# Kernel tuning notes

Measured on AMD Instinct MI355X. Metric: run time of the kernel, lower is better.

## Reference

```python
import jax, jax.numpy as jnp
import numpy as np
import math

N_HEADS = 12  # from init_kwargs


def setup_inputs() -> dict:
    key = jax.random.key(0)
    ks = jax.random.split(key, 9)
    B, N, D = 32, 577, 768
    s = 1.0 / math.sqrt(D)
    return {
        "x": jax.random.normal(ks[0], (B, N, D), jnp.float32),
        "Wq": jax.random.normal(ks[1], (D, D), jnp.float32) * s,
        "bq": jax.random.normal(ks[2], (D,), jnp.float32) * 0.02,
        "Wk": jax.random.normal(ks[3], (D, D), jnp.float32) * s,
        "bk": jax.random.normal(ks[4], (D,), jnp.float32) * 0.02,
        "Wv": jax.random.normal(ks[5], (D, D), jnp.float32) * s,
        "bv": jax.random.normal(ks[6], (D,), jnp.float32) * 0.02,
        "Wo": jax.random.normal(ks[7], (D, D), jnp.float32) * s,
        "bo": jax.random.normal(ks[8], (D,), jnp.float32) * 0.02,
    }


def reference(x, Wq, bq, Wk, bk, Wv, bv, Wo, bo):
    B, N, D = x.shape
    H = N_HEADS
    Hd = D // H
    # project then split heads (intended semantics of the torch module)
    q = (x @ Wq.T + bq).reshape(B, N, H, Hd)
    k = (x @ Wk.T + bk).reshape(B, N, H, Hd)
    v = (x @ Wv.T + bv).reshape(B, N, H, Hd)
    # NOTE: faithful quirk - scale by sqrt(d_size), not sqrt(head_dim)
    scores = jnp.einsum('bqhd,bkhd->bhqk', q, k) / math.sqrt(D)  # [B,H,N,N]
    # faithful quirk: mask = triu(ones); positions where mask==0 (strictly
    # lower triangle, k < q) are filled with float32 min -> anti-causal mask
    allowed = jnp.triu(jnp.ones((N, N), dtype=bool))
    scores = jnp.where(allowed, scores, jnp.finfo(jnp.float32).min)
    att = jax.nn.softmax(scores, axis=3)  # dropout p=0.0 -> identity
    out = jnp.einsum('bhqk,bkhd->bqhd', att, v).reshape(B, N, D)
    return out @ Wo.T + bo
```

## Files before the change

### kernel.cpp

```cpp
#include <hip/hip_runtime.h>
#include <cstdint>
#include <cstddef>


typedef __bf16 bf16;
typedef __bf16 bf16x4 __attribute__((ext_vector_type(4)));
typedef __bf16 bf16x8 __attribute__((ext_vector_type(8)));
typedef float  f32x4  __attribute__((ext_vector_type(4)));

#define DEVI __device__ __forceinline__

constexpr int BATCH = 32;
constexpr int NSEQ  = 577;
constexpr int DMODEL= 768;
constexpr int NHEAD = 12;
constexpr int HD    = 64;
constexpr int M_ROWS = BATCH * NSEQ;
constexpr int M_PAD  = 145 * 128;
constexpr int N_PAD  = 640;
constexpr int QKV_N  = 3 * DMODEL;
constexpr float QSCALE = 0.036084391824351615f * 1.4426950408889634f;

DEVI void async_copy16(const void* g, void* l) {
  void* gg = (void*)(uintptr_t)g;
  __builtin_amdgcn_global_load_lds(
      (__attribute__((address_space(1))) void*)gg,
      (__attribute__((address_space(3))) void*)l,
      16, 0, 0);
}

DEVI f32x4 mfma16(bf16x8 a, bf16x8 b, f32x4 c) {
  return __builtin_amdgcn_mfma_f32_16x16x32_bf16(a, b, c, 0, 0, 0);
}

__global__ __launch_bounds__(256) void cast_kernel(
    const float* __restrict__ x,
    const float* __restrict__ wq, const float* __restrict__ wk,
    const float* __restrict__ wv, const float* __restrict__ wo,
    bf16* __restrict__ xb, bf16* __restrict__ wcat, bf16* __restrict__ wob)
{
  constexpr int XQ = (M_ROWS * DMODEL) / 4;
  constexpr int WQ = (DMODEL * DMODEL) / 4;
  int idx = blockIdx.x * 256 + threadIdx.x;
  const float4* src; bf16* dst; int off;
  if (idx < XQ) { src = (const float4*)x; dst = xb; off = idx; }
  else {
    int u = idx - XQ; int w = u / WQ; off = u - w * WQ;
    src = (const float4*)(w == 0 ? wq : w == 1 ? wk : w == 2 ? wv : wo);
    dst = (w < 3) ? (wcat + (size_t)w * DMODEL * DMODEL) : wob;
  }
  float4 v = src[off];
  bf16x4 o;
  o[0] = (bf16)v.x; o[1] = (bf16)v.y; o[2] = (bf16)v.z; o[3] = (bf16)v.w;
  *(bf16x4*)(dst + (size_t)off * 4) = o;
}

template <int MODE>
__global__ __launch_bounds__(256) void gemm_bt(
    const bf16* __restrict__ A, const bf16* __restrict__ Bw,
    const float* __restrict__ bias0, const float* __restrict__ bias1,
    const float* __restrict__ bias2,
    float* __restrict__ Cout,
    bf16* __restrict__ Qb, bf16* __restrict__ Kb, bf16* __restrict__ Vtb)
{
  __shared__ __align__(16) bf16 As[128 * 64];
  __shared__ __align__(16) bf16 Bs[128 * 64];
  const int t = threadIdx.x;
  const int w = t >> 6, lane = t & 63;
  const int g = lane >> 4, cl = lane & 15;
  const int wm = (w >> 1) * 64, wn = (w & 1) * 64;
  const int m0 = blockIdx.y * 128, n0 = blockIdx.x * 128;

  f32x4 acc[4][4] = {};

  const int srow = t >> 3;
  const int scol = ((t & 7) ^ (srow & 7)) * 8;
  const bf16* Ag = A  + (size_t)(m0 + srow) * 768 + scol;
  const bf16* Bg = Bw + (size_t)(n0 + srow) * 768 + scol;
  char* lA = (char*)As + w * 1024;
  char* lB = (char*)Bs + w * 1024;

  for (int kb = 0; kb < 768; kb += 64) {
#pragma unroll
    for (int c = 0; c < 4; ++c) {
      async_copy16(Ag + kb + (size_t)c * 32 * 768, lA + c * 4096);
      async_copy16(Bg + kb + (size_t)c * 32 * 768, lB + c * 4096);
    }
    __syncthreads();
#pragma unroll
    for (int ks = 0; ks < 2; ++ks) {
      const int ch = ((ks * 4 + g) ^ (cl & 7)) * 8;
      bf16x8 af[4], bfr[4];
#pragma unroll
      for (int i = 0; i < 4; ++i)
        af[i] = *(const bf16x8*)(As + (wm + i * 16 + cl) * 64 + ch);
#pragma unroll
      for (int j = 0; j < 4; ++j)
        bfr[j] = *(const bf16x8*)(Bs + (wn + j * 16 + cl) * 64 + ch);
#pragma unroll
      for (int i = 0; i < 4; ++i)
#pragma unroll
        for (int j = 0; j < 4; ++j)
          acc[i][j] = mfma16(af[i], bfr[j], acc[i][j]);
    }
    __syncthreads();
  }

  if constexpr (MODE == 0) {
#pragma unroll
    for (int j = 0; j < 4; ++j) {
      const int n = n0 + wn + j * 16 + cl;
      const int which = n >= 1536 ? 2 : (n >= 768 ? 1 : 0);
      const int rem = n - which * 768;
      const int h = rem >> 6, d = rem & 63;
      const float bias = (which == 0 ? bias0 : which == 1 ? bias1 : bias2)[rem];
#pragma unroll
      for (int i = 0; i < 4; ++i) {
#pragma unroll
        for (int r = 0; r < 4; ++r) {
          const unsigned m = (unsigned)(m0 + wm + i * 16 + g * 4 + r);
          if (m >= (unsigned)M_ROWS) continue;
          const unsigned bb = m / 577u;
          const unsigned nq = m - bb * 577u;
          const float fv = acc[i][j][r] + bias;
          if (which == 0)
            Qb[((size_t)(bb * NHEAD + h) * N_PAD + nq) * HD + d] = (bf16)(fv * QSCALE);
          else if (which == 1)
            Kb[((size_t)(bb * NHEAD + h) * N_PAD + nq) * HD + d] = (bf16)fv;
          else
            Vtb[((size_t)(bb * NHEAD + h) * HD + d) * N_PAD + nq] = (bf16)fv;
        }
      }
    }
  } else {
#pragma unroll
    for (int j = 0; j < 4; ++j) {
      const int n = n0 + wn + j * 16 + cl;
      const float bias = bias0[n];
#pragma unroll
      for (int i = 0; i < 4; ++i) {
#pragma unroll
        for (int r = 0; r < 4; ++r) {
          const unsigned m = (unsigned)(m0 + wm + i * 16 + g * 4 + r);
          if (m < (unsigned)M_ROWS)
            Cout[(size_t)m * 768 + n] = acc[i][j][r] + bias;
        }
      }
    }
  }
}

__global__ __launch_bounds__(256) void attn_kernel(
    const bf16* __restrict__ Qb, const bf16* __restrict__ Kb,
    const bf16* __restrict__ Vtb, bf16* __restrict__ Ao)
{
  __shared__ __align__(16) bf16 Qs[64 * 64];
  __shared__ __align__(16) bf16 Ks[64 * 64];
  __shared__ __align__(16) bf16 Vs[64 * 64];
  __shared__ __align__(16) bf16 Ps[4 * 16 * 64];

  const int t = threadIdx.x, w = t >> 6, lane = t & 63;
  const int g = lane >> 4, cl = lane & 15;
  const int qb = blockIdx.x;
  const int bh = blockIdx.y;
  const size_t kqbase = (size_t)bh * (N_PAD * HD);
  const size_t vbase  = (size_t)bh * (HD * N_PAD);

  const int srow = t >> 3;
  const int scol = ((t & 7) ^ (srow & 7)) * 8;

  {
    const bf16* Qg = Qb + kqbase + (size_t)(qb * 64 + srow) * HD + scol;
    async_copy16(Qg,           (char*)Qs + w * 1024);
    async_copy16(Qg + 32 * HD, (char*)Qs + 4096 + w * 1024);
  }

  f32x4 oacc[4] = {};
  f32x4 lsum = {};
  bf16x8 onesf;
#pragma unroll
  for (int e = 0; e < 8; ++e) onesf[e] = (bf16)(cl == 0 ? 1.0f : 0.0f);

  const int q0 = qb * 64 + w * 16 + g * 4;
  const bf16* Kg = Kb  + kqbase + (size_t)srow * HD + scol;
  const bf16* Vg = Vtb + vbase  + (size_t)srow * N_PAD + scol;
  bf16* pw = Ps + w * 1024;

  for (int jb = qb; jb < 10; ++jb) {
    async_copy16(Kg + (size_t)jb * 64 * HD,            (char*)Ks + w * 1024);
    async_copy16(Kg + (size_t)(jb * 64 + 32) * HD,     (char*)Ks + 4096 + w * 1024);
    async_copy16(Vg + jb * 64,                         (char*)Vs + w * 1024);
    async_copy16(Vg + jb * 64 + (size_t)32 * N_PAD,    (char*)Vs + 4096 + w * 1024);
    __syncthreads();

    f32x4 s[4] = {};
#pragma unroll
    for (int ks = 0; ks < 2; ++ks) {
      const int ch = ((ks * 4 + g) ^ (cl & 7)) * 8;
      bf16x8 aq = *(const bf16x8*)(Qs + (w * 16 + cl) * 64 + ch);
#pragma unroll
      for (int j = 0; j < 4; ++j) {
        bf16x8 bk = *(const bf16x8*)(Ks + (j * 16 + cl) * 64 + ch);
        s[j] = mfma16(aq, bk, s[j]);
      }
    }

    float p[4][4];
    if (jb == qb || jb == 9) {
#pragma unroll
      for (int j = 0; j < 4; ++j) {
        const int kg = jb * 64 + j * 16 + cl;
#pragma unroll
        for (int r = 0; r < 4; ++r) {
          const bool ok = (kg >= q0 + r) && (kg < NSEQ);
          p[j][r] = ok ? exp2f(s[j][r]) : 0.f;
        }
      }
    } else {
#pragma unroll
      for (int j = 0; j < 4; ++j)
#pragma unroll
        for (int r = 0; r < 4; ++r)
          p[j][r] = exp2f(s[j][r]);
    }

#pragma unroll
    for (int j = 0; j < 4; ++j)
#pragma unroll
      for (int r = 0; r < 4; ++r) {
        const int row = g * 4 + r;
        const int col = j * 16 + cl;
        pw[row * 64 + ((col >> 3) ^ (row & 7)) * 8 + (col & 7)] = (bf16)p[j][r];
      }

#pragma unroll
    for (int ks = 0; ks < 2; ++ks) {
      const int ch = ((ks * 4 + g) ^ (cl & 7)) * 8;
      bf16x8 ap = *(const bf16x8*)(pw + cl * 64 + ch);
#pragma unroll
      for (int j = 0; j < 4; ++j) {
        bf16x8 bv = *(const bf16x8*)(Vs + (j * 16 + cl) * 64 + ch);
        oacc[j] = mfma16(ap, bv, oacc[j]);
      }
      lsum = mfma16(ap, onesf, lsum);
    }
    __syncthreads();
  }

  const int b_ = bh / NHEAD, h_ = bh - (bh / NHEAD) * NHEAD;
#pragma unroll
  for (int r = 0; r < 4; ++r) {
    const int qg = q0 + r;
    const float l = __shfl(lsum[r], lane & 48, 64);
    if (qg >= NSEQ) continue;
    const float inv = 1.f / l;
    const size_t row = ((size_t)b_ * NSEQ + qg) * DMODEL + h_ * HD;
#pragma unroll
    for (int j = 0; j < 4; ++j)
      Ao[row + j * 16 + cl] = (bf16)(oacc[j][r] * inv);
  }
}

extern "C" void kernel_launch(void* const* d_in, const int* in_sizes, int n_in,
                              void* d_out, int out_size, void* d_ws, size_t ws_size,
                              hipStream_t stream) {
  const float* x  = (const float*)d_in[0];
  const float* Wq = (const float*)d_in[1];
  const float* bq = (const float*)d_in[2];
  const float* Wk = (const float*)d_in[3];
  const float* bk = (const float*)d_in[4];
  const float* Wv = (const float*)d_in[5];
  const float* bv = (const float*)d_in[6];
  const float* Wo = (const float*)d_in[7];
  const float* bo = (const float*)d_in[8];

  char* ws = (char*)d_ws;
  size_t off = 0;
  auto alloc = [&](size_t bytes) -> char* {
    char* p = ws + off;
    off += (bytes + 255) & ~(size_t)255;
    return p;
  };
  bf16* xb   = (bf16*)alloc((size_t)M_PAD * DMODEL * 2);
  bf16* wcat = (bf16*)alloc((size_t)QKV_N * DMODEL * 2);
  bf16* wob  = (bf16*)alloc((size_t)DMODEL * DMODEL * 2);
  bf16* Qb   = (bf16*)alloc((size_t)BATCH * NHEAD * N_PAD * HD * 2);
  bf16* Kb   = (bf16*)alloc((size_t)BATCH * NHEAD * N_PAD * HD * 2);
  bf16* Vtb  = (bf16*)alloc((size_t)BATCH * NHEAD * HD * N_PAD * 2);
  bf16* Ao   = (bf16*)alloc((size_t)M_PAD * DMODEL * 2);
  (void)ws_size; (void)in_sizes; (void)n_in; (void)out_size;

  constexpr int XQ = (M_ROWS * DMODEL) / 4;
  constexpr int WQ = (DMODEL * DMODEL) / 4;
  const int cast_blocks = (XQ + 4 * WQ) / 256;
  cast_kernel<<<cast_blocks, 256, 0, stream>>>(x, Wq, Wk, Wv, Wo, xb, wcat, wob);

  gemm_bt<0><<<dim3(QKV_N / 128, M_PAD / 128), 256, 0, stream>>>(
      xb, wcat, bq, bk, bv, nullptr, Qb, Kb, Vtb);

  attn_kernel<<<dim3(10, BATCH * NHEAD), 256, 0, stream>>>(Qb, Kb, Vtb, Ao);

  gemm_bt<1><<<dim3(DMODEL / 128, M_PAD / 128), 256, 0, stream>>>(
      Ao, wob, bo, nullptr, nullptr, (float*)d_out, nullptr, nullptr, nullptr);
}
```

Measured before the change: 400.3 us.

## Use 128-query attention tiles with double-buffered K/V and halve GEMM K-step

```diff
diff --git a/kernel.cpp b/kernel.cpp
--- a/kernel.cpp
+++ b/kernel.cpp
@@ -63,8 +63,8 @@
     float* __restrict__ Cout,
     bf16* __restrict__ Qb, bf16* __restrict__ Kb, bf16* __restrict__ Vtb)
 {
-  __shared__ __align__(16) bf16 As[128 * 64];
-  __shared__ __align__(16) bf16 Bs[128 * 64];
+  __shared__ __align__(16) bf16 As[128 * 32];
+  __shared__ __align__(16) bf16 Bs[128 * 32];
   const int t = threadIdx.x;
   const int w = t >> 6, lane = t & 63;
   const int g = lane >> 4, cl = lane & 15;
@@ -73,36 +73,29 @@
 
   f32x4 acc[4][4] = {};
 
-  const int srow = t >> 3;
-  const int scol = ((t & 7) ^ (srow & 7)) * 8;
-  const bf16* Ag = A  + (size_t)(m0 + srow) * 768 + scol;
-  const bf16* Bg = Bw + (size_t)(n0 + srow) * 768 + scol;
+  const bf16* Ag = A  + (size_t)(m0 + (t >> 2)) * 768 + (t & 3) * 8;
+  const bf16* Bg = Bw + (size_t)(n0 + (t >> 2)) * 768 + (t & 3) * 8;
   char* lA = (char*)As + w * 1024;
   char* lB = (char*)Bs + w * 1024;
 
-  for (int kb = 0; kb < 768; kb += 64) {
-#pragma unroll
-    for (int c = 0; c < 4; ++c) {
-      async_copy16(Ag + kb + (size_t)c * 32 * 768, lA + c * 4096);
-      async_copy16(Bg + kb + (size_t)c * 32 * 768, lB + c * 4096);
-    }
+  for (int kb = 0; kb < 768; kb += 32) {
+    async_copy16(Ag + kb,                    lA);
+    async_copy16(Ag + kb + (size_t)64 * 768, lA + 4096);
+    async_copy16(Bg + kb,                    lB);
+    async_copy16(Bg + kb + (size_t)64 * 768, lB + 4096);
     __syncthreads();
-#pragma unroll
-    for (int ks = 0; ks < 2; ++ks) {
-      const int ch = ((ks * 4 + g) ^ (cl & 7)) * 8;
-      bf16x8 af[4], bfr[4];
-#pragma unroll
-      for (int i = 0; i < 4; ++i)
-        af[i] = *(const bf16x8*)(As + (wm + i * 16 + cl) * 64 + ch);
+    bf16x8 af[4], bfr[4];
+#pragma unroll
+    for (int i = 0; i < 4; ++i)
+      af[i] = *(const bf16x8*)(As + (wm + i * 16 + cl) * 32 + g * 8);
+#pragma unroll
+    for (int j = 0; j < 4; ++j)
+      bfr[j] = *(const bf16x8*)(Bs + (wn + j * 16 + cl) * 32 + g * 8);
+#pragma unroll
+    for (int i = 0; i < 4; ++i)
 #pragma unroll
       for (int j = 0; j < 4; ++j)
-        bfr[j] = *(const bf16x8*)(Bs + (wn + j * 16 + cl) * 64 + ch);
-#pragma unroll
-      for (int i = 0; i < 4; ++i)
-#pragma unroll
-        for (int j = 0; j < 4; ++j)
-          acc[i][j] = mfma16(af[i], bfr[j], acc[i][j]);
-    }
+        acc[i][j] = mfma16(af[i], bfr[j], acc[i][j]);
     __syncthreads();
   }
 
@@ -154,14 +147,14 @@
     const bf16* __restrict__ Qb, const bf16* __restrict__ Kb,
     const bf16* __restrict__ Vtb, bf16* __restrict__ Ao)
 {
-  __shared__ __align__(16) bf16 Qs[64 * 64];
-  __shared__ __align__(16) bf16 Ks[64 * 64];
-  __shared__ __align__(16) bf16 Vs[64 * 64];
-  __shared__ __align__(16) bf16 Ps[4 * 16 * 64];
+  __shared__ __align__(16) bf16 Qs[128 * 64];
+  __shared__ __align__(16) bf16 Ks[2][64 * 64];
+  __shared__ __align__(16) bf16 Vs[2][64 * 64];
+  __shared__ __align__(16) bf16 Ps[4 * 32 * 64];
 
   const int t = threadIdx.x, w = t >> 6, lane = t & 63;
   const int g = lane >> 4, cl = lane & 15;
-  const int qb = blockIdx.x;
+  const int qt = blockIdx.x;
   const int bh = blockIdx.y;
   const size_t kqbase = (size_t)bh * (N_PAD * HD);
   const size_t vbase  = (size_t)bh * (HD * N_PAD);
@@ -169,96 +162,124 @@
   const int srow = t >> 3;
   const int scol = ((t & 7) ^ (srow & 7)) * 8;
 
-  {
-    const bf16* Qg = Qb + kqbase + (size_t)(qb * 64 + srow) * HD + scol;
-    async_copy16(Qg,           (char*)Qs + w * 1024);
-    async_copy16(Qg + 32 * HD, (char*)Qs + 4096 + w * 1024);
-  }
-
-  f32x4 oacc[4] = {};
-  f32x4 lsum = {};
-  bf16x8 onesf;
-#pragma unroll
-  for (int e = 0; e < 8; ++e) onesf[e] = (bf16)(cl == 0 ? 1.0f : 0.0f);
-
-  const int q0 = qb * 64 + w * 16 + g * 4;
+  const bf16* Qg = Qb  + kqbase + (size_t)(qt * 128 + srow) * HD + scol;
   const bf16* Kg = Kb  + kqbase + (size_t)srow * HD + scol;
   const bf16* Vg = Vtb + vbase  + (size_t)srow * N_PAD + scol;
-  bf16* pw = Ps + w * 1024;
-
-  for (int jb = qb; jb < 10; ++jb) {
-    async_copy16(Kg + (size_t)jb * 64 * HD,            (char*)Ks + w * 1024);
-    async_copy16(Kg + (size_t)(jb * 64 + 32) * HD,     (char*)Ks + 4096 + w * 1024);
-    async_copy16(Vg + jb * 64,                         (char*)Vs + w * 1024);
-    async_copy16(Vg + jb * 64 + (size_t)32 * N_PAD,    (char*)Vs + 4096 + w * 1024);
-    __syncthreads();
-
-    f32x4 s[4] = {};
+
+  const int jb0 = 2 * qt, nit = 10 - jb0;
+
+#pragma unroll
+  for (int c = 0; c < 4; ++c)
+    async_copy16(Qg + (size_t)c * 32 * HD, (char*)Qs + c * 4096 + w * 1024);
+#pragma unroll
+  for (int c = 0; c < 2; ++c) {
+    async_copy16(Kg + (size_t)(jb0 * 64 + c * 32) * HD,  (char*)Ks[0] + c * 4096 + w * 1024);
+    async_copy16(Vg + jb0 * 64 + (size_t)(c * 32) * N_PAD, (char*)Vs[0] + c * 4096 + w * 1024);
+  }
+  __syncthreads();
+
+  f32x4 oacc[2][4] = {};
+  f32x4 lsum[2] = {};
+  bf16x8 onesf;
+#pragma unroll
+  for (int e = 0; e < 8; ++e) onesf[e] = (bf16)(cl == 0 ? 1.0f : 0.0f);
+
+  bf16* pw = Ps + w * 2048;
+  const int qw0 = qt * 128 + w * 32;
+
+  for (int it = 0; it < nit; ++it) {
+    const int jb = jb0 + it;
+    const int buf = it & 1;
+    if (it + 1 < nit) {
+      const int jn = jb + 1, nb = buf ^ 1;
+#pragma unroll
+      for (int c = 0; c < 2; ++c) {
+        async_copy16(Kg + (size_t)(jn * 64 + c * 32) * HD,   (char*)Ks[nb] + c * 4096 + w * 1024);
+        async_copy16(Vg + jn * 64 + (size_t)(c * 32) * N_PAD, (char*)Vs[nb] + c * 4096 + w * 1024);
+      }
+    }
+
+    f32x4 s[2][4] = {};
 #pragma unroll
     for (int ks = 0; ks < 2; ++ks) {
       const int ch = ((ks * 4 + g) ^ (cl & 7)) * 8;
-      bf16x8 aq = *(const bf16x8*)(Qs + (w * 16 + cl) * 64 + ch);
-#pragma unroll
-      for (int j = 0; j < 4; ++j) {
-        bf16x8 bk = *(const bf16x8*)(Ks + (j * 16 + cl) * 64 + ch);
-        s[j] = mfma16(aq, bk, s[j]);
-      }
-    }
-
-    float p[4][4];
-    if (jb == qb || jb == 9) {
-#pragma unroll
-      for (int j = 0; j < 4; ++j) {
-        const int kg = jb * 64 + j * 16 + cl;
+#pragma unroll
+      for (int f = 0; f < 2; ++f) {
+        bf16x8 aq = *(const bf16x8*)(Qs + (w * 32 + f * 16 + cl) * 64 + ch);
+#pragma unroll
+        for (int j = 0; j < 4; ++j) {
+          bf16x8 bk = *(const bf16x8*)(Ks[buf] + (j * 16 + cl) * 64 + ch);
+          s[f][j] = mfma16(aq, bk, s[f][j]);
+        }
+      }
+    }
+
+    float p[2][4][4];
+    const bool need_mask = (jb * 64 < qw0 + 32) || (jb == 9);
+    if (need_mask) {
+#pragma unroll
+      for (int f = 0; f < 2; ++f)
+#pragma unroll
+        for (int j = 0; j < 4; ++j) {
+          const int kg = jb * 64 + j * 16 + cl;
+#pragma unroll
+          for (int r = 0; r < 4; ++r) {
+            const bool ok = (kg >= qw0 + f * 16 + g * 4 + r) && (kg < NSEQ);
+            p[f][j][r] = ok ? exp2f(s[f][j][r]) : 0.f;
+          }
+        }
+    } else {
+#pragma unroll
+      for (int f = 0; f < 2; ++f)
+#pragma unroll
+        for (int j = 0; j < 4; ++j)
+#pragma unroll
+          for (int r = 0; r < 4; ++r)
+            p[f][j][r] = exp2f(s[f][j][r]);
+    }
+
+#pragma unroll
+    for (int f = 0; f < 2; ++f)
+#pragma unroll
+      for (int j = 0; j < 4; ++j)
 #pragma unroll
         for (int r = 0; r < 4; ++r) {
-          const bool ok = (kg >= q0 + r) && (kg < NSEQ);
-          p[j][r] = ok ? exp2f(s[j][r]) : 0.f;
-        }
-      }
-    } else {
-#pragma unroll
-      for (int j = 0; j < 4; ++j)
-#pragma unroll
-        for (int r = 0; r < 4; ++r)
-          p[j][r] = exp2f(s[j][r]);
-    }
-
-#pragma unroll
-    for (int j = 0; j < 4; ++j)
-#pragma unroll
-      for (int r = 0; r < 4; ++r) {
-        const int row = g * 4 + r;
-        const int col = j * 16 + cl;
-        pw[row * 64 + ((col >> 3) ^ (row & 7)) * 8 + (col & 7)] = (bf16)p[j][r];
-      }
+          const int row = f * 16 + g * 4 + r;
+          const int col = j * 16 + cl;
+          pw[row * 64 + ((col >> 3) ^ (row & 7)) * 8 + (col & 7)] = (bf16)p[f][j][r];
+        }
 
 #pragma unroll
     for (int ks = 0; ks < 2; ++ks) {
       const int ch = ((ks * 4 + g) ^ (cl & 7)) * 8;
-      bf16x8 ap = *(const bf16x8*)(pw + cl * 64 + ch);
-#pragma unroll
-      for (int j = 0; j < 4; ++j) {
-        bf16x8 bv = *(const bf16x8*)(Vs + (j * 16 + cl) * 64 + ch);
-        oacc[j] = mfma16(ap, bv, oacc[j]);
-      }
-      lsum = mfma16(ap, onesf, lsum);
+#pragma unroll
+      for (int f = 0; f < 2; ++f) {
+        bf16x8 ap = *(const bf16x8*)(pw + (f * 16 + cl) * 64 + ch);
+#pragma unroll
+        for (int j = 0; j < 4; ++j) {
+          bf16x8 bv = *(const bf16x8*)(Vs[buf] + (j * 16 + cl) * 64 + ch);
+          oacc[f][j] = mfma16(ap, bv, oacc[f][j]);
+        }
+        lsum[f] = mfma16(ap, onesf, lsum[f]);
+      }
     }
     __syncthreads();
   }
 
   const int b_ = bh / NHEAD, h_ = bh - (bh / NHEAD) * NHEAD;
 #pragma unroll
-  for (int r = 0; r < 4; ++r) {
-    const int qg = q0 + r;
-    const float l = __shfl(lsum[r], lane & 48, 64);
-    if (qg >= NSEQ) continue;
-    const float inv = 1.f / l;
-    const size_t row = ((size_t)b_ * NSEQ + qg) * DMODEL + h_ * HD;
-#pragma unroll
-    for (int j = 0; j < 4; ++j)
-      Ao[row + j * 16 + cl] = (bf16)(oacc[j][r] * inv);
-  }
+  for (int f = 0; f < 2; ++f)
+#pragma unroll
+    for (int r = 0; r < 4; ++r) {
+      const int qg = qw0 + f * 16 + g * 4 + r;
+      const float l = __shfl(lsum[f][r], lane & 48, 64);
+      if (qg >= NSEQ) continue;
+      const float inv = 1.f / l;
+      const size_t row = ((size_t)b_ * NSEQ + qg) * DMODEL + h_ * HD;
+#pragma unroll
+      for (int j = 0; j < 4; ++j)
+        Ao[row + j * 16 + cl] = (bf16)(oacc[f][j][r] * inv);
+    }
 }
 
 extern "C" void kernel_launch(void* const* d_in, const int* in_sizes, int n_in,
@@ -298,7 +319,7 @@
   gemm_bt<0><<<dim3(QKV_N / 128, M_PAD / 128), 256, 0, stream>>>(
       xb, wcat, bq, bk, bv, nullptr, Qb, Kb, Vtb);
 
-  attn_kernel<<<dim3(10, BATCH * NHEAD), 256, 0, stream>>>(Qb, Kb, Vtb, Ao);
+  attn_kernel<<<dim3(5, BATCH * NHEAD), 256, 0, stream>>>(Qb, Kb, Vtb, Ao);
 
   gemm_bt<1><<<dim3(DMODEL / 128, M_PAD / 128), 256, 0, stream>>>(
       Ao, wob, bo, nullptr, nullptr, (float*)d_out, nullptr, nullptr, nullptr);
```

Result: no change. 395.4 us (-1.2%).
